# Performance work log

Measured on AMD Instinct MI355X. Metric: run time of the kernel, lower is better.

## Reference

```python
import jax, jax.numpy as jnp
import numpy as np

B, L, I, H, O = 32, 4096, 128, 256, 128
DELAY = 4  # delay-line length is DELAY+1


def setup_inputs() -> dict:
    key = jax.random.key(0)
    ks = jax.random.split(key, 9)
    s = 0.02
    return {
        "x": jax.random.normal(ks[0], (B, L, I), jnp.float32),
        # MGRUCell params (minimal-GRU: forget gate uses delayed state)
        "Wz": jax.random.normal(ks[1], (I, H), jnp.float32) * s,
        "Uz": jax.random.normal(ks[2], (H, H), jnp.float32) * s,
        "bz": jnp.zeros((H,), jnp.float32),
        "Wh": jax.random.normal(ks[3], (I, H), jnp.float32) * s,
        "Uh": jax.random.normal(ks[4], (H, H), jnp.float32) * s,
        "bh": jnp.zeros((H,), jnp.float32),
        # head: Linear(H, O)
        "Wo": jax.random.normal(ks[5], (H, O), jnp.float32) * s,
        "bo": jnp.zeros((O,), jnp.float32),
    }


def reference(x, Wz, Uz, bz, Wh, Uh, bh, Wo, bo):
    Bv, Lv, _ = x.shape
    Hv = Wz.shape[1]
    # precompute all input projections in two big GEMMs (time-parallel part)
    xz = jnp.einsum("bli,ih->blh", x, Wz) + bz  # [B,L,H]
    xh = jnp.einsum("bli,ih->blh", x, Wh) + bh  # [B,L,H]
    h0 = jnp.zeros((Bv, Hv), x.dtype)
    hist0 = jnp.zeros((DELAY + 1, Bv, Hv), x.dtype)  # delay line, hist[0] is oldest

    def step(carry, xs):
        h, hist = carry
        xz_t, xh_t = xs
        h_delay = hist[0]
        z = jax.nn.sigmoid(xz_t + h_delay @ Uz)          # gate from delayed state
        h_tilde = jnp.tanh(xh_t + (z * h) @ Uh)           # candidate (minimal-GRU)
        h_new = (1.0 - z) * h + z * h_tilde
        hist_new = jnp.concatenate([hist[1:], h_new[None]], axis=0)
        return (h_new, hist_new), h_new

    (_, _), hs = jax.lax.scan(
        step, (h0, hist0), (jnp.swapaxes(xz, 0, 1), jnp.swapaxes(xh, 0, 1))
    )  # hs: [L,B,H]
    # per-step Linear head, applied as one GEMM over all steps
    y = jnp.einsum("lbh,ho->blo", hs, Wo) + bo  # [B,L,O]
    return y
```

## Files before the change

kernel.cpp:

```cpp
#include <hip/hip_runtime.h>
#include <hip/hip_bf16.h>

typedef _Float16 half2v __attribute__((ext_vector_type(2)));
typedef _Float16 half8v __attribute__((ext_vector_type(8)));
typedef float float4v __attribute__((ext_vector_type(4)));
typedef unsigned int u32;
typedef unsigned short u16;

#define DEV static __device__ __forceinline__

DEV u32 pack2(float a, float b) {
  half2v h = { (_Float16)a, (_Float16)b };
  return __builtin_bit_cast(u32, h);
}
DEV half2v uph(u32 u) { return __builtin_bit_cast(half2v, u); }
DEV u16 ftoh16(float f) { return __builtin_bit_cast(u16, (_Float16)f); }
DEV float h16tof(u16 s) { return (float)__builtin_bit_cast(_Float16, s); }

#if __has_builtin(__builtin_amdgcn_fdot2)
DEV float fdot2(half2v a, half2v b, float c) { return __builtin_amdgcn_fdot2(a, b, c, false); }
#else
DEV float fdot2(half2v a, half2v b, float c) {
  return c + (float)a.x * (float)b.x + (float)a.y * (float)b.y;
}
#endif

DEV float fast_rcp(float x) { return __builtin_amdgcn_rcpf(x); }
DEV float sigmoid_f(float x) { return fast_rcp(1.f + exp2f(-1.4426950408889634f * x)); }
DEV float tanh_f(float x) {
  float e = exp2f(x * 2.8853900817779268f);
  return 1.f - 2.f * fast_rcp(e + 1.f);
}

DEV void barrier_lgkm() {
  __asm__ __volatile__("s_waitcnt lgkmcnt(0)\ns_barrier" ::: "memory");
}

__global__ void prep_transpose(const float* __restrict__ Wz, const float* __restrict__ Wh,
                               const float* __restrict__ Wo, _Float16* __restrict__ Wzt,
                               _Float16* __restrict__ Wht, _Float16* __restrict__ Wot)
{
  const float* src; _Float16* dst; int R, C;
  if (blockIdx.y == 0)      { src = Wz; dst = Wzt; R = 128; C = 256; }
  else if (blockIdx.y == 1) { src = Wh; dst = Wht; R = 128; C = 256; }
  else                      { src = Wo; dst = Wot; R = 256; C = 128; }
  int total = R * C;
  for (int idx = blockIdx.x * blockDim.x + threadIdx.x; idx < total;
       idx += gridDim.x * blockDim.x) {
    int rr = idx / C, cc = idx % C;
    dst[(size_t)cc * R + rr] = (_Float16)src[idx];
  }
}

template <int K, int N, bool A_F32, bool OUT_F16>
__global__ __launch_bounds__(256, 2) void gemm_mfma(
    const void* __restrict__ A_, const _Float16* __restrict__ Bt,
    const float* __restrict__ bias, void* __restrict__ out)
{
  __shared__ _Float16 Blds[N * K];

  const int tid = threadIdx.x;
  constexpr int CHUNKS = K / 8;
  constexpr int ITER = (N * K / 8) / 256;
#pragma unroll
  for (int i = 0; i < ITER; ++i) {
    int idx = tid + i * 256;
    int n = idx / CHUNKS;
    int c = idx % CHUNKS;
    int cs = c ^ (n & 7);
    *(uint4*)(Blds + (size_t)n * K + cs * 8) =
        *(const uint4*)(Bt + (size_t)n * K + c * 8);
  }
  __syncthreads();

  const int w = tid >> 6, l = tid & 63;
  const int lm = l & 15, lq = l >> 4;
  const size_t m0 = (size_t)blockIdx.x * 128;

  float4v acc[2][N / 16] = {};

#pragma unroll
  for (int kk = 0; kk < K / 32; ++kk) {
    const int kbase = kk * 32 + lq * 8;
    half8v af[2];
#pragma unroll
    for (int ms = 0; ms < 2; ++ms) {
      const size_t row = m0 + (size_t)(w * 2 + ms) * 16 + lm;
      if constexpr (A_F32) {
        const float* ap = (const float*)A_ + row * K + kbase;
        float4 x0 = *(const float4*)ap;
        float4 x1 = *(const float4*)(ap + 4);
        af[ms] = half8v{(_Float16)x0.x, (_Float16)x0.y, (_Float16)x0.z, (_Float16)x0.w,
                        (_Float16)x1.x, (_Float16)x1.y, (_Float16)x1.z, (_Float16)x1.w};
      } else {
        af[ms] = *(const half8v*)((const _Float16*)A_ + row * K + kbase);
      }
    }
    const int c = kk * 4 + lq;
#pragma unroll
    for (int nt = 0; nt < N / 16; ++nt) {
      const int n = nt * 16 + lm;
      half8v bf = *(const half8v*)(Blds + (size_t)n * K + (c ^ (lm & 7)) * 8);
      acc[0][nt] = __builtin_amdgcn_mfma_f32_16x16x32_f16(af[0], bf, acc[0][nt], 0, 0, 0);
      acc[1][nt] = __builtin_amdgcn_mfma_f32_16x16x32_f16(af[1], bf, acc[1][nt], 0, 0, 0);
    }
  }

#pragma unroll
  for (int ms = 0; ms < 2; ++ms) {
    const size_t rowbase = m0 + (size_t)(w * 2 + ms) * 16 + lq * 4;
#pragma unroll
    for (int nt = 0; nt < N / 16; ++nt) {
      const int col = nt * 16 + lm;
      const float bcol = bias[col];
#pragma unroll
      for (int rr = 0; rr < 4; ++rr) {
        const size_t row = rowbase + rr;
        float v = acc[ms][nt][rr] + bcol;
        if constexpr (OUT_F16) ((_Float16*)out)[row * N + col] = (_Float16)v;
        else                   ((float*)out)[row * N + col] = v;
      }
    }
  }
}

__global__ __launch_bounds__(512, 2) void scan_kernel(
    const u32* __restrict__ xz32, const u32* __restrict__ xh32,
    const float* __restrict__ Uz, const float* __restrict__ Uh,
    u32* __restrict__ hsOut)
{
  const int b   = blockIdx.x;
  const int tid = threadIdx.x;
  const int w   = tid >> 6;
  const int l   = tid & 63;
  const int g   = w >> 2;
  const int wv  = w & 3;

  __shared__ __align__(16) u16 histS[8][264];
  __shared__ __align__(16) u16 zringS[8][264];
  __shared__ __align__(16) u16 zhS[8][264];
  __shared__ __align__(16) u16 xhS[2][1024];
  __shared__ __align__(16) u16 xzS[2][1024];

  uint4 W[32];

  const size_t xb32 = (size_t)b * 4096 * 128;
  const u16* xz16v = (const u16*)xz32;
  const int c   = wv * 64 + l;
  const int rr  = c >> 6;
  const int c4  = (c & 63) * 4;

  {
    const float* U = (g == 0) ? Uh : Uz;
    const int lm = l & 15, lo = (l >> 4) * 8;
#pragma unroll
    for (int kt = 0; kt < 8; ++kt)
#pragma unroll
      for (int nt = 0; nt < 4; ++nt) {
        u32 q[4];
#pragma unroll
        for (int p2 = 0; p2 < 4; ++p2) {
          int k0 = kt * 32 + lo + 2 * p2;
          int cn = wv * 64 + nt * 16 + lm;
          q[p2] = pack2(U[(size_t)k0 * 256 + cn], U[(size_t)(k0 + 1) * 256 + cn]);
        }
        W[kt * 4 + nt] = make_uint4(q[0], q[1], q[2], q[3]);
      }
  }

  for (int i = tid; i < 4 * 264; i += 512) (&histS[4][0])[i] = 0;
  for (int i = tid; i < 264; i += 512) zhS[0][i] = 0;

  if (g == 1) {
    uint2 xzv = *(const uint2*)&xz16v[((size_t)b * 4096 + rr) * 256 + c4];
    half2v a0 = uph(xzv.x), a1 = uph(xzv.y);
    u32 z01 = pack2(sigmoid_f((float)a0.x), sigmoid_f((float)a0.y));
    u32 z23 = pack2(sigmoid_f((float)a1.x), sigmoid_f((float)a1.y));
    *(uint2*)&zringS[rr][c4] = make_uint2(z01, z23);
    *(uint2*)&xhS[0][rr * 256 + c4] =
        *(const uint2*)&xh32[xb32 + (size_t)rr * 128 + (c & 63) * 2];
    *(uint2*)&xzS[0][rr * 256 + c4] =
        *(const uint2*)&xz16v[((size_t)b * 4096 + 4 + rr) * 256 + c4];
  }
  float h = 0.f;
  __syncthreads();

  const int koff = (l >> 4) * 8;
  const int q    = l >> 4;

  for (int tb = 0; tb < 4096; tb += 4) {
    const int p = (tb >> 2) & 1;
    uint2 xhv, xzv2;
#pragma unroll
    for (int u = 0; u < 4; ++u) {
      const int t = tb + u;
      if (g == 0) {
        const u16* zrow = &zhS[t & 7][0];
        float xh_t = h16tof(xhS[p][u * 256 + c]);
        float z_t  = h16tof(zringS[t & 7][c]);
        float4v acc4[4] = {};
#pragma unroll
        for (int kt = 0; kt < 8; ++kt) {
          half8v a = __builtin_bit_cast(
              half8v, *(const uint4*)&zrow[kt * 32 + koff]);
#pragma unroll
          for (int nt = 0; nt < 4; ++nt)
            acc4[nt] = __builtin_amdgcn_mfma_f32_16x16x32_f16(
                a, __builtin_bit_cast(half8v, W[kt * 4 + nt]), acc4[nt], 0, 0, 0);
        }
        float pre = q == 0 ? acc4[0][0] : q == 1 ? acc4[1][0]
                  : q == 2 ? acc4[2][0] : acc4[3][0];
        float htl = tanh_f(pre + xh_t);
        h += z_t * (htl - h);
        histS[t & 7][c] = ftoh16(h);
        if (u < 3) {
          float zn = h16tof(zringS[(t + 1) & 7][c]);
          zhS[(t + 1) & 7][c] = ftoh16(zn * h);
        }
        barrier_lgkm();
        if (u == 3) {
          float zn = h16tof(zringS[(t + 1) & 7][c]);
          zhS[(t + 1) & 7][c] = ftoh16(zn * h);
          barrier_lgkm();
        }
      } else {
        if (u == 0) {
          int rh = tb + 4 + rr; if (rh > 4095) rh = 4095;
          xhv = *(const uint2*)&xh32[xb32 + (size_t)rh * 128 + (c & 63) * 2];
          int rz = tb + 8 + rr; if (rz > 4095) rz = 4095;
          xzv2 = *(const uint2*)&xz16v[((size_t)b * 4096 + rz) * 256 + c4];
          if (tb > 0) {
            int ro = tb - 4 + rr;
            uint2 hv = *(const uint2*)&histS[ro & 7][c4];
            *(uint2*)&hsOut[xb32 + (size_t)ro * 128 + (c & 63) * 2] = hv;
          }
          barrier_lgkm();
        } else if (u == 2) {
          *(uint2*)&xhS[p ^ 1][rr * 256 + c4] = xhv;
          *(uint2*)&xzS[p ^ 1][rr * 256 + c4] = xzv2;
          barrier_lgkm();
        } else if (u == 3) {
          const int srow = (tb + 7 + (l & 3)) & 7;
          float4v acc4[4] = {};
#pragma unroll
          for (int kt = 0; kt < 8; ++kt) {
            half8v a = __builtin_bit_cast(
                half8v, *(const uint4*)&histS[srow][kt * 32 + koff]);
#pragma unroll
            for (int nt = 0; nt < 4; ++nt)
              acc4[nt] = __builtin_amdgcn_mfma_f32_16x16x32_f16(
                  a, __builtin_bit_cast(half8v, W[kt * 4 + nt]), acc4[nt], 0, 0, 0);
          }
          {
            const int lm16 = l & 15;
#pragma unroll
            for (int nt = 0; nt < 4; ++nt) {
              float4v a = acc4[nt];
              float pre = q == 0 ? a[0] : q == 1 ? a[1] : q == 2 ? a[2] : a[3];
              int cn = wv * 64 + nt * 16 + lm16;
              float zv = sigmoid_f(pre + h16tof(xzS[p][q * 256 + cn]));
              zringS[(tb + 4 + q) & 7][cn] = ftoh16(zv);
            }
          }
          barrier_lgkm();
          barrier_lgkm();
        } else {
          barrier_lgkm();
        }
      }
    }
  }

  if (g == 1) {
    int ro = 4092 + rr;
    uint2 hv = *(const uint2*)&histS[ro & 7][c4];
    *(uint2*)&hsOut[xb32 + (size_t)ro * 128 + (c & 63) * 2] = hv;
  }
}

extern "C" void kernel_launch(void* const* d_in, const int* in_sizes, int n_in,
                              void* d_out, int out_size, void* d_ws, size_t ws_size,
                              hipStream_t stream)
{
  (void)in_sizes; (void)n_in; (void)out_size; (void)ws_size;
  const float* x  = (const float*)d_in[0];
  const float* Wz = (const float*)d_in[1];
  const float* Uz = (const float*)d_in[2];
  const float* bz = (const float*)d_in[3];
  const float* Wh = (const float*)d_in[4];
  const float* Uh = (const float*)d_in[5];
  const float* bh = (const float*)d_in[6];
  const float* Wo = (const float*)d_in[7];
  const float* bo = (const float*)d_in[8];

  char* ws = (char*)d_ws;
  _Float16* Wzt  = (_Float16*)(ws);
  _Float16* Wht  = (_Float16*)(ws + (64 << 10));
  _Float16* Wot  = (_Float16*)(ws + (128 << 10));
  _Float16* xz16 = (_Float16*)(ws + (256 << 10));
  _Float16* xh16 = (_Float16*)(ws + (256 << 10) + (size_t)64 * 1024 * 1024);

  _Float16* hs16 = (_Float16*)d_out;

  prep_transpose<<<dim3(32, 3), 256, 0, stream>>>(Wz, Wh, Wo, Wzt, Wht, Wot);
  gemm_mfma<128, 256, true, true><<<1024, 256, 0, stream>>>(x, Wzt, bz, xz16);
  gemm_mfma<128, 256, true, true><<<1024, 256, 0, stream>>>(x, Wht, bh, xh16);
  scan_kernel<<<32, 512, 0, stream>>>((const u32*)xz16, (const u32*)xh16,
                                      Uz, Uh, (u32*)d_out);
  gemm_mfma<256, 128, false, false><<<1024, 256, 0, stream>>>(hs16, Wot, bo, d_out);
}
```

Before: 2.741 ms.

## Compute z*h on the fly at block start to drop a barrier; split MFMA chains

At the first step of each 4-step block, the h-path warps now form the z*h operand directly from zring and the previous history row instead of reading a precomputed zh row. This removes the extra write and barrier at the end of each block, and the z-path warps drop a matching barrier so the two groups stay in step. Both MFMA reductions are split into two independent accumulator chains (k 0-3 and 4-7) that are summed afterwards, which shortens the dependent MFMA latency chain. The cost is extra LDS reads and packed fp16 multiplies at u==0, and rounding changes slightly because z*h is now formed in fp16 from fp16 h.

```diff
diff --git a/kernel.cpp b/kernel.cpp
--- a/kernel.cpp
+++ b/kernel.cpp
@@ -16,14 +16,6 @@
 DEV half2v uph(u32 u) { return __builtin_bit_cast(half2v, u); }
 DEV u16 ftoh16(float f) { return __builtin_bit_cast(u16, (_Float16)f); }
 DEV float h16tof(u16 s) { return (float)__builtin_bit_cast(_Float16, s); }
-
-#if __has_builtin(__builtin_amdgcn_fdot2)
-DEV float fdot2(half2v a, half2v b, float c) { return __builtin_amdgcn_fdot2(a, b, c, false); }
-#else
-DEV float fdot2(half2v a, half2v b, float c) {
-  return c + (float)a.x * (float)b.x + (float)a.y * (float)b.y;
-}
-#endif
 
 DEV float fast_rcp(float x) { return __builtin_amdgcn_rcpf(x); }
 DEV float sigmoid_f(float x) { return fast_rcp(1.f + exp2f(-1.4426950408889634f * x)); }
@@ -157,19 +149,18 @@
     for (int kt = 0; kt < 8; ++kt)
 #pragma unroll
       for (int nt = 0; nt < 4; ++nt) {
-        u32 q[4];
+        u32 q2[4];
 #pragma unroll
         for (int p2 = 0; p2 < 4; ++p2) {
           int k0 = kt * 32 + lo + 2 * p2;
           int cn = wv * 64 + nt * 16 + lm;
-          q[p2] = pack2(U[(size_t)k0 * 256 + cn], U[(size_t)(k0 + 1) * 256 + cn]);
+          q2[p2] = pack2(U[(size_t)k0 * 256 + cn], U[(size_t)(k0 + 1) * 256 + cn]);
         }
-        W[kt * 4 + nt] = make_uint4(q[0], q[1], q[2], q[3]);
+        W[kt * 4 + nt] = make_uint4(q2[0], q2[1], q2[2], q2[3]);
       }
   }
 
   for (int i = tid; i < 4 * 264; i += 512) (&histS[4][0])[i] = 0;
-  for (int i = tid; i < 264; i += 512) zhS[0][i] = 0;
 
   if (g == 1) {
     uint2 xzv = *(const uint2*)&xz16v[((size_t)b * 4096 + rr) * 256 + c4];
@@ -195,34 +186,62 @@
     for (int u = 0; u < 4; ++u) {
       const int t = tb + u;
       if (g == 0) {
-        const u16* zrow = &zhS[t & 7][0];
         float xh_t = h16tof(xhS[p][u * 256 + c]);
         float z_t  = h16tof(zringS[t & 7][c]);
-        float4v acc4[4] = {};
-#pragma unroll
-        for (int kt = 0; kt < 8; ++kt) {
-          half8v a = __builtin_bit_cast(
-              half8v, *(const uint4*)&zrow[kt * 32 + koff]);
-#pragma unroll
-          for (int nt = 0; nt < 4; ++nt)
-            acc4[nt] = __builtin_amdgcn_mfma_f32_16x16x32_f16(
-                a, __builtin_bit_cast(half8v, W[kt * 4 + nt]), acc4[nt], 0, 0, 0);
+        u16 zn_u = (u < 3) ? zringS[(t + 1) & 7][c] : (u16)0;
+
+        float4v accA[4] = {}, accB[4] = {};
+        if (u == 0) {
+          const u16* zrow = &zringS[t & 7][0];
+          const u16* hrow = &histS[(t + 7) & 7][0];
+#pragma unroll
+          for (int kt = 0; kt < 4; ++kt) {
+            half8v az = __builtin_bit_cast(half8v, *(const uint4*)&zrow[kt * 32 + koff]);
+            half8v ah = __builtin_bit_cast(half8v, *(const uint4*)&hrow[kt * 32 + koff]);
+            half8v a = az * ah;
+#pragma unroll
+            for (int nt = 0; nt < 4; ++nt)
+              accA[nt] = __builtin_amdgcn_mfma_f32_16x16x32_f16(
+                  a, __builtin_bit_cast(half8v, W[kt * 4 + nt]), accA[nt], 0, 0, 0);
+          }
+#pragma unroll
+          for (int kt = 4; kt < 8; ++kt) {
+            half8v az = __builtin_bit_cast(half8v, *(const uint4*)&zrow[kt * 32 + koff]);
+            half8v ah = __builtin_bit_cast(half8v, *(const uint4*)&hrow[kt * 32 + koff]);
+            half8v a = az * ah;
+#pragma unroll
+            for (int nt = 0; nt < 4; ++nt)
+              accB[nt] = __builtin_amdgcn_mfma_f32_16x16x32_f16(
+                  a, __builtin_bit_cast(half8v, W[kt * 4 + nt]), accB[nt], 0, 0, 0);
+          }
+        } else {
+          const u16* zhrow = &zhS[t & 7][0];
+#pragma unroll
+          for (int kt = 0; kt < 4; ++kt) {
+            half8v a = __builtin_bit_cast(half8v, *(const uint4*)&zhrow[kt * 32 + koff]);
+#pragma unroll
+            for (int nt = 0; nt < 4; ++nt)
+              accA[nt] = __builtin_amdgcn_mfma_f32_16x16x32_f16(
+                  a, __builtin_bit_cast(half8v, W[kt * 4 + nt]), accA[nt], 0, 0, 0);
+          }
+#pragma unroll
+          for (int kt = 4; kt < 8; ++kt) {
+            half8v a = __builtin_bit_cast(half8v, *(const uint4*)&zhrow[kt * 32 + koff]);
+#pragma unroll
+            for (int nt = 0; nt < 4; ++nt)
+              accB[nt] = __builtin_amdgcn_mfma_f32_16x16x32_f16(
+                  a, __builtin_bit_cast(half8v, W[kt * 4 + nt]), accB[nt], 0, 0, 0);
+          }
         }
-        float pre = q == 0 ? acc4[0][0] : q == 1 ? acc4[1][0]
-                  : q == 2 ? acc4[2][0] : acc4[3][0];
-        float htl = tanh_f(pre + xh_t);
+        float preA = q == 0 ? accA[0][0] : q == 1 ? accA[1][0]
+                   : q == 2 ? accA[2][0] : accA[3][0];
+        float preB = q == 0 ? accB[0][0] : q == 1 ? accB[1][0]
+                   : q == 2 ? accB[2][0] : accB[3][0];
+        float htl = tanh_f(preA + preB + xh_t);
         h += z_t * (htl - h);
         histS[t & 7][c] = ftoh16(h);
-        if (u < 3) {
-          float zn = h16tof(zringS[(t + 1) & 7][c]);
-          zhS[(t + 1) & 7][c] = ftoh16(zn * h);
-        }
+        if (u < 3) zhS[(t + 1) & 7][c] = ftoh16(h16tof(zn_u) * h);
         barrier_lgkm();
-        if (u == 3) {
-          float zn = h16tof(zringS[(t + 1) & 7][c]);
-          zhS[(t + 1) & 7][c] = ftoh16(zn * h);
-          barrier_lgkm();
-        }
       } else {
         if (u == 0) {
           int rh = tb + 4 + rr; if (rh > 4095) rh = 4095;
@@ -241,28 +260,36 @@
           barrier_lgkm();
         } else if (u == 3) {
           const int srow = (tb + 7 + (l & 3)) & 7;
-          float4v acc4[4] = {};
-#pragma unroll
-          for (int kt = 0; kt < 8; ++kt) {
+          float4v accA[4] = {}, accB[4] = {};
+#pragma unroll
+          for (int kt = 0; kt < 4; ++kt) {
             half8v a = __builtin_bit_cast(
                 half8v, *(const uint4*)&histS[srow][kt * 32 + koff]);
 #pragma unroll
             for (int nt = 0; nt < 4; ++nt)
-              acc4[nt] = __builtin_amdgcn_mfma_f32_16x16x32_f16(
-                  a, __builtin_bit_cast(half8v, W[kt * 4 + nt]), acc4[nt], 0, 0, 0);
+              accA[nt] = __builtin_amdgcn_mfma_f32_16x16x32_f16(
+                  a, __builtin_bit_cast(half8v, W[kt * 4 + nt]), accA[nt], 0, 0, 0);
+          }
+#pragma unroll
+          for (int kt = 4; kt < 8; ++kt) {
+            half8v a = __builtin_bit_cast(
+                half8v, *(const uint4*)&histS[srow][kt * 32 + koff]);
+#pragma unroll
+            for (int nt = 0; nt < 4; ++nt)
+              accB[nt] = __builtin_amdgcn_mfma_f32_16x16x32_f16(
+                  a, __builtin_bit_cast(half8v, W[kt * 4 + nt]), accB[nt], 0, 0, 0);
           }
           {
             const int lm16 = l & 15;
 #pragma unroll
             for (int nt = 0; nt < 4; ++nt) {
-              float4v a = acc4[nt];
-              float pre = q == 0 ? a[0] : q == 1 ? a[1] : q == 2 ? a[2] : a[3];
+              float4v s = accA[nt] + accB[nt];
+              float pre = q == 0 ? s[0] : q == 1 ? s[1] : q == 2 ? s[2] : s[3];
               int cn = wv * 64 + nt * 16 + lm16;
               float zv = sigmoid_f(pre + h16tof(xzS[p][q * 256 + cn]));
               zringS[(tb + 4 + q) & 7][cn] = ftoh16(zv);
             }
           }
-          barrier_lgkm();
           barrier_lgkm();
         } else {
           barrier_lgkm();
```

Result: no change. 2.789 ms (+1.7%).

## Halve scan block to 4 fat waves each owning 128 columns

Applied to the files above, without the earlier changes.

The recurrent scan kernel drops from 8 waves to 4. Each wave now holds twice as many weight fragments in registers (64 uint4) and computes 8 MFMA column tiles, with two hidden units per lane. Global load/store duties move into all waves instead of a dedicated group. This reduces barrier participants and per-step synchronisation cost, but doubles the serial MFMA chain per wave on the critical path and raises register pressure.

```diff
diff --git a/kernel.cpp b/kernel.cpp
--- a/kernel.cpp
+++ b/kernel.cpp
@@ -16,14 +16,6 @@
 DEV half2v uph(u32 u) { return __builtin_bit_cast(half2v, u); }
 DEV u16 ftoh16(float f) { return __builtin_bit_cast(u16, (_Float16)f); }
 DEV float h16tof(u16 s) { return (float)__builtin_bit_cast(_Float16, s); }
-
-#if __has_builtin(__builtin_amdgcn_fdot2)
-DEV float fdot2(half2v a, half2v b, float c) { return __builtin_amdgcn_fdot2(a, b, c, false); }
-#else
-DEV float fdot2(half2v a, half2v b, float c) {
-  return c + (float)a.x * (float)b.x + (float)a.y * (float)b.y;
-}
-#endif
 
 DEV float fast_rcp(float x) { return __builtin_amdgcn_rcpf(x); }
 DEV float sigmoid_f(float x) { return fast_rcp(1.f + exp2f(-1.4426950408889634f * x)); }
@@ -124,7 +116,7 @@
   }
 }
 
-__global__ __launch_bounds__(512, 2) void scan_kernel(
+__global__ __launch_bounds__(256, 1) void scan_kernel(
     const u32* __restrict__ xz32, const u32* __restrict__ xh32,
     const float* __restrict__ Uz, const float* __restrict__ Uh,
     u32* __restrict__ hsOut)
@@ -133,8 +125,8 @@
   const int tid = threadIdx.x;
   const int w   = tid >> 6;
   const int l   = tid & 63;
-  const int g   = w >> 2;
-  const int wv  = w & 3;
+  const int fat = w >> 1;
+  const int wh  = w & 1;
 
   __shared__ __align__(16) u16 histS[8][264];
   __shared__ __align__(16) u16 zringS[8][264];
@@ -142,51 +134,51 @@
   __shared__ __align__(16) u16 xhS[2][1024];
   __shared__ __align__(16) u16 xzS[2][1024];
 
-  uint4 W[32];
+  uint4 W[64];
 
   const size_t xb32 = (size_t)b * 4096 * 128;
   const u16* xz16v = (const u16*)xz32;
-  const int c   = wv * 64 + l;
-  const int rr  = c >> 6;
-  const int c4  = (c & 63) * 4;
+  const int rr  = tid >> 6;
+  const int c4  = (tid & 63) * 4;
+  const int lm  = l & 15;
+  const int q   = l >> 4;
+  const int koff = q * 8;
+  const int c0  = wh * 128 + l;
+  const int c1  = c0 + 64;
 
   {
-    const float* U = (g == 0) ? Uh : Uz;
-    const int lm = l & 15, lo = (l >> 4) * 8;
+    const float* U = (fat == 0) ? Uh : Uz;
 #pragma unroll
     for (int kt = 0; kt < 8; ++kt)
 #pragma unroll
-      for (int nt = 0; nt < 4; ++nt) {
-        u32 q[4];
+      for (int nt = 0; nt < 8; ++nt) {
+        u32 q2[4];
 #pragma unroll
         for (int p2 = 0; p2 < 4; ++p2) {
-          int k0 = kt * 32 + lo + 2 * p2;
-          int cn = wv * 64 + nt * 16 + lm;
-          q[p2] = pack2(U[(size_t)k0 * 256 + cn], U[(size_t)(k0 + 1) * 256 + cn]);
-        }
-        W[kt * 4 + nt] = make_uint4(q[0], q[1], q[2], q[3]);
-      }
-  }
-
-  for (int i = tid; i < 4 * 264; i += 512) (&histS[4][0])[i] = 0;
-  for (int i = tid; i < 264; i += 512) zhS[0][i] = 0;
-
-  if (g == 1) {
+          int k0 = kt * 32 + koff + 2 * p2;
+          int cn = wh * 128 + nt * 16 + lm;
+          q2[p2] = pack2(U[(size_t)k0 * 256 + cn], U[(size_t)(k0 + 1) * 256 + cn]);
+        }
+        W[kt * 8 + nt] = make_uint4(q2[0], q2[1], q2[2], q2[3]);
+      }
+  }
+
+  for (int i = tid; i < 4 * 264; i += 256) (&histS[4][0])[i] = 0;
+  for (int i = tid; i < 264; i += 256) zhS[0][i] = 0;
+
+  {
     uint2 xzv = *(const uint2*)&xz16v[((size_t)b * 4096 + rr) * 256 + c4];
     half2v a0 = uph(xzv.x), a1 = uph(xzv.y);
     u32 z01 = pack2(sigmoid_f((float)a0.x), sigmoid_f((float)a0.y));
     u32 z23 = pack2(sigmoid_f((float)a1.x), sigmoid_f((float)a1.y));
     *(uint2*)&zringS[rr][c4] = make_uint2(z01, z23);
     *(uint2*)&xhS[0][rr * 256 + c4] =
-        *(const uint2*)&xh32[xb32 + (size_t)rr * 128 + (c & 63) * 2];
+        *(const uint2*)&xh32[xb32 + (size_t)rr * 128 + (tid & 63) * 2];
     *(uint2*)&xzS[0][rr * 256 + c4] =
         *(const uint2*)&xz16v[((size_t)b * 4096 + 4 + rr) * 256 + c4];
   }
-  float h = 0.f;
+  float h0 = 0.f, h1 = 0.f;
   __syncthreads();
-
-  const int koff = (l >> 4) * 8;
-  const int q    = l >> 4;
 
   for (int tb = 0; tb < 4096; tb += 4) {
     const int p = (tb >> 2) & 1;
@@ -194,73 +186,82 @@
 #pragma unroll
     for (int u = 0; u < 4; ++u) {
       const int t = tb + u;
-      if (g == 0) {
-        const u16* zrow = &zhS[t & 7][0];
-        float xh_t = h16tof(xhS[p][u * 256 + c]);
-        float z_t  = h16tof(zringS[t & 7][c]);
-        float4v acc4[4] = {};
+
+      if (u == 0) {
+        int rh = tb + 4 + rr; if (rh > 4095) rh = 4095;
+        xhv = *(const uint2*)&xh32[xb32 + (size_t)rh * 128 + (tid & 63) * 2];
+        int rz = tb + 8 + rr; if (rz > 4095) rz = 4095;
+        xzv2 = *(const uint2*)&xz16v[((size_t)b * 4096 + rz) * 256 + c4];
+        if (tb > 0) {
+          int ro = tb - 4 + rr;
+          uint2 hv = *(const uint2*)&histS[ro & 7][c4];
+          *(uint2*)&hsOut[xb32 + (size_t)ro * 128 + (tid & 63) * 2] = hv;
+        }
+      } else if (u == 2) {
+        *(uint2*)&xhS[p ^ 1][rr * 256 + c4] = xhv;
+        *(uint2*)&xzS[p ^ 1][rr * 256 + c4] = xzv2;
+      }
+
+      if (fat == 0) {
+        float xh_t0 = h16tof(xhS[p][u * 256 + c0]);
+        float xh_t1 = h16tof(xhS[p][u * 256 + c1]);
+        float z_t0  = h16tof(zringS[t & 7][c0]);
+        float z_t1  = h16tof(zringS[t & 7][c1]);
+        const u16* zhrow = &zhS[t & 7][0];
+        float4v acc4[8] = {};
 #pragma unroll
         for (int kt = 0; kt < 8; ++kt) {
           half8v a = __builtin_bit_cast(
-              half8v, *(const uint4*)&zrow[kt * 32 + koff]);
-#pragma unroll
-          for (int nt = 0; nt < 4; ++nt)
+              half8v, *(const uint4*)&zhrow[kt * 32 + koff]);
+#pragma unroll
+          for (int nt = 0; nt < 8; ++nt)
             acc4[nt] = __builtin_amdgcn_mfma_f32_16x16x32_f16(
-                a, __builtin_bit_cast(half8v, W[kt * 4 + nt]), acc4[nt], 0, 0, 0);
-        }
-        float pre = q == 0 ? acc4[0][0] : q == 1 ? acc4[1][0]
-                  : q == 2 ? acc4[2][0] : acc4[3][0];
-        float htl = tanh_f(pre + xh_t);
-        h += z_t * (htl - h);
-        histS[t & 7][c] = ftoh16(h);
+                a, __builtin_bit_cast(half8v, W[kt * 8 + nt]), acc4[nt], 0, 0, 0);
+        }
+        float pre0 = q == 0 ? acc4[0][0] : q == 1 ? acc4[1][0]
+                   : q == 2 ? acc4[2][0] : acc4[3][0];
+        float pre1 = q == 0 ? acc4[4][0] : q == 1 ? acc4[5][0]
+                   : q == 2 ? acc4[6][0] : acc4[7][0];
+        float htl0 = tanh_f(pre0 + xh_t0);
+        float htl1 = tanh_f(pre1 + xh_t1);
+        h0 += z_t0 * (htl0 - h0);
+        h1 += z_t1 * (htl1 - h1);
+        histS[t & 7][c0] = ftoh16(h0);
+        histS[t & 7][c1] = ftoh16(h1);
         if (u < 3) {
-          float zn = h16tof(zringS[(t + 1) & 7][c]);
-          zhS[(t + 1) & 7][c] = ftoh16(zn * h);
+          float zn0 = h16tof(zringS[(t + 1) & 7][c0]);
+          float zn1 = h16tof(zringS[(t + 1) & 7][c1]);
+          zhS[(t + 1) & 7][c0] = ftoh16(zn0 * h0);
+          zhS[(t + 1) & 7][c1] = ftoh16(zn1 * h1);
         }
         barrier_lgkm();
         if (u == 3) {
-          float zn = h16tof(zringS[(t + 1) & 7][c]);
-          zhS[(t + 1) & 7][c] = ftoh16(zn * h);
+          float zn0 = h16tof(zringS[(t + 1) & 7][c0]);
+          float zn1 = h16tof(zringS[(t + 1) & 7][c1]);
+          zhS[(t + 1) & 7][c0] = ftoh16(zn0 * h0);
+          zhS[(t + 1) & 7][c1] = ftoh16(zn1 * h1);
           barrier_lgkm();
         }
       } else {
-        if (u == 0) {
-          int rh = tb + 4 + rr; if (rh > 4095) rh = 4095;
-          xhv = *(const uint2*)&xh32[xb32 + (size_t)rh * 128 + (c & 63) * 2];
-          int rz = tb + 8 + rr; if (rz > 4095) rz = 4095;
-          xzv2 = *(const uint2*)&xz16v[((size_t)b * 4096 + rz) * 256 + c4];
-          if (tb > 0) {
-            int ro = tb - 4 + rr;
-            uint2 hv = *(const uint2*)&histS[ro & 7][c4];
-            *(uint2*)&hsOut[xb32 + (size_t)ro * 128 + (c & 63) * 2] = hv;
-          }
-          barrier_lgkm();
-        } else if (u == 2) {
-          *(uint2*)&xhS[p ^ 1][rr * 256 + c4] = xhv;
-          *(uint2*)&xzS[p ^ 1][rr * 256 + c4] = xzv2;
-          barrier_lgkm();
-        } else if (u == 3) {
+        if (u == 3) {
           const int srow = (tb + 7 + (l & 3)) & 7;
-          float4v acc4[4] = {};
+          float4v acc4[8] = {};
 #pragma unroll
           for (int kt = 0; kt < 8; ++kt) {
             half8v a = __builtin_bit_cast(
                 half8v, *(const uint4*)&histS[srow][kt * 32 + koff]);
 #pragma unroll
-            for (int nt = 0; nt < 4; ++nt)
+            for (int nt = 0; nt < 8; ++nt)
               acc4[nt] = __builtin_amdgcn_mfma_f32_16x16x32_f16(
-                  a, __builtin_bit_cast(half8v, W[kt * 4 + nt]), acc4[nt], 0, 0, 0);
+                  a, __builtin_bit_cast(half8v, W[kt * 8 + nt]), acc4[nt], 0, 0, 0);
           }
-          {
-            const int lm16 = l & 15;
-#pragma unroll
-            for (int nt = 0; nt < 4; ++nt) {
-              float4v a = acc4[nt];
-              float pre = q == 0 ? a[0] : q == 1 ? a[1] : q == 2 ? a[2] : a[3];
-              int cn = wv * 64 + nt * 16 + lm16;
-              float zv = sigmoid_f(pre + h16tof(xzS[p][q * 256 + cn]));
-              zringS[(tb + 4 + q) & 7][cn] = ftoh16(zv);
-            }
+#pragma unroll
+          for (int nt = 0; nt < 8; ++nt) {
+            float4v a = acc4[nt];
+            float pre = q == 0 ? a[0] : q == 1 ? a[1] : q == 2 ? a[2] : a[3];
+            int cn = wh * 128 + nt * 16 + lm;
+            float zv = sigmoid_f(pre + h16tof(xzS[p][q * 256 + cn]));
+            zringS[(tb + 4 + q) & 7][cn] = ftoh16(zv);
           }
           barrier_lgkm();
           barrier_lgkm();
@@ -271,10 +272,10 @@
     }
   }
 
-  if (g == 1) {
+  {
     int ro = 4092 + rr;
     uint2 hv = *(const uint2*)&histS[ro & 7][c4];
-    *(uint2*)&hsOut[xb32 + (size_t)ro * 128 + (c & 63) * 2] = hv;
+    *(uint2*)&hsOut[xb32 + (size_t)ro * 128 + (tid & 63) * 2] = hv;
   }
 }
 
@@ -305,7 +306,7 @@
   prep_transpose<<<dim3(32, 3), 256, 0, stream>>>(Wz, Wh, Wo, Wzt, Wht, Wot);
   gemm_mfma<128, 256, true, true><<<1024, 256, 0, stream>>>(x, Wzt, bz, xz16);
   gemm_mfma<128, 256, true, true><<<1024, 256, 0, stream>>>(x, Wht, bh, xh16);
-  scan_kernel<<<32, 512, 0, stream>>>((const u32*)xz16, (const u32*)xh16,
+  scan_kernel<<<32, 256, 0, stream>>>((const u32*)xz16, (const u32*)xh16,
                                       Uz, Uh, (u32*)d_out);
   gemm_mfma<256, 128, false, false><<<1024, 256, 0, stream>>>(hs16, Wot, bo, d_out);
 }
```

New measurement: 4.738 ms. 72.8% more time.
